# Kernel tuning notes

Hardware: AMD Instinct MI355X
Metric: run time of the kernel (lower is better)

## Reference

```python
import jax, jax.numpy as jnp
import numpy as np

B, T, U, D = 2, 512, 48, 512
H, K = 1024, 128  # hidden_channels, num_classes; fc1 in = 2*D = 1024


def setup_inputs() -> dict:
    key = jax.random.key(0)
    ks = jax.random.split(key, 9)
    s = 0.02
    return {
        "img_feature": jax.random.normal(ks[0], (B, T, D), jnp.float32),
        "label_feature": jax.random.normal(ks[1], (B, U, D), jnp.float32),
        "masks": jnp.ones((B, 1, T), jnp.float32),
        "W1": jax.random.normal(ks[2], (H, 2 * D), jnp.float32) * s,
        "b1": jnp.zeros((H,), jnp.float32),
        "W2": jax.random.normal(ks[3], (K, H), jnp.float32) * s,
        "b2": jnp.zeros((K,), jnp.float32),
        "conv_w": jax.random.normal(ks[4], (K, D), jnp.float32) * s,
        "conv_b": jnp.zeros((K,), jnp.float32),
    }


def reference(img_feature, label_feature, masks, W1, b1, W2, b2, conv_w, conv_b):
    # pointwise Conv1d over img features: (B,T,D) -> (B,K,T), masked
    img_seg_score = (jnp.einsum('btd,kd->bkt', img_feature, conv_w)
                     + conv_b[None, :, None]) * masks
    # fc1(cat(label, img)) == label @ Wl^T + img @ Wi^T + b1 (broadcast add),
    # avoiding the O(B*U*T*2D) repeat+cat intermediate.
    d = label_feature.shape[-1]
    Wl, Wi = W1[:, :d], W1[:, d:]
    lab = jnp.einsum('bud,hd->buh', label_feature, Wl)  # (B,U,H)
    img = jnp.einsum('btd,hd->bth', img_feature, Wi)    # (B,T,H)
    h = jnp.tanh(lab[:, :, None, :] + img[:, None, :, :] + b1)  # (B,U,T,H)
    joint = jnp.einsum('buth,kh->butk', h, W2) + b2
    joint_score = jax.nn.log_softmax(joint, axis=-1)
    return (img_seg_score, joint_score)
```

## Files before the change

kernel.cpp:

```cpp
#include <hip/hip_runtime.h>
#include <math.h>

#define BB 2
#define TT 512
#define UU 48
#define DD 512
#define HH 1024
#define KK 128

typedef _Float16 f16x8 __attribute__((ext_vector_type(8)));
typedef __fp16 fp16x2_t __attribute__((ext_vector_type(2)));
typedef float floatx4 __attribute__((ext_vector_type(4)));

__device__ __forceinline__ f16x8 tanh8z(f16x8 z) {
    f16x8 o;
#pragma unroll
    for (int i = 0; i < 8; i += 2) {
        float e0 = __builtin_amdgcn_exp2f((float)z[i]);
        float e1 = __builtin_amdgcn_exp2f((float)z[i + 1]);
        float r0 = __builtin_amdgcn_rcpf(e0 + 1.0f);
        float r1 = __builtin_amdgcn_rcpf(e1 + 1.0f);
        fp16x2_t p = __builtin_amdgcn_cvt_pkrtz(fmaf(-2.0f, r0, 1.0f),
                                                fmaf(-2.0f, r1, 1.0f));
        o[i] = (_Float16)p[0];
        o[i + 1] = (_Float16)p[1];
    }
    return o;
}

__global__ __launch_bounds__(256) void mid_kernel5(
    const float* __restrict__ img, const float* __restrict__ labf,
    const float* __restrict__ W1, const float* __restrict__ W2,
    const float* __restrict__ conv_w,
    const float* __restrict__ b1, const float* __restrict__ conv_b,
    const float* __restrict__ masks,
    _Float16* __restrict__ imgHf, _Float16* __restrict__ labHf,
    _Float16* __restrict__ W2s, float* __restrict__ seg_out) {
    int bid = blockIdx.x, tid = threadIdx.x;
    if (bid >= 624) {
        int base = (bid - 624) * 256 + tid;
#pragma unroll
        for (int i = 0; i < 32; ++i) {
            int o = base + i * 4096;
            int hg = o >> 10, kk2 = (o >> 3) & 127, hl = o & 7;
            W2s[o] = (_Float16)W2[(size_t)kk2 * HH + hg * 8 + hl];
        }
        return;
    }
    __shared__ __align__(16) _Float16 a_s[32][72];
    __shared__ __align__(16) _Float16 w_s[4096];
    const float* Arow;
    const float* Wbase;
    int r0, n0b, wstride, region;
    if (bid < 512) {
        region = 0; Arow = img; Wbase = W1 + 512; wstride = 2 * DD;
        int xcd = bid & 7, j = bid >> 3;
        r0 = (j & 31) * 32; n0b = (xcd * 2 + (j >> 5)) * 64;
    } else if (bid < 560) {
        region = 1; Arow = labf; Wbase = W1; wstride = 2 * DD;
        int i = bid - 512; r0 = (i % 3) * 32; n0b = (i / 3) * 64;
    } else {
        region = 2; Arow = img; Wbase = conv_w; wstride = DD;
        int i = bid - 560; r0 = (i >> 1) * 32; n0b = (i & 1) * 64;
    }
    int lane = tid & 63, wv = tid >> 6;
    int m0 = (wv & 1) * 16, n0w = (wv >> 1) * 32;
    int q = lane >> 4, r = lane & 15;
    int arow = tid >> 3, acol = (tid & 7) * 8;
    int wn = tid >> 2, wk0 = (tid & 3) * 16;
    const float* aptr = &Arow[(size_t)(r0 + arow) * DD + acol];
    const float* wptr = &Wbase[(size_t)(n0b + wn) * wstride + wk0];
    floatx4 acc[2] = {};
    float4 pa0, pa1, pw[4];
    pa0 = *(const float4*)aptr;
    pa1 = *(const float4*)(aptr + 4);
#pragma unroll
    for (int i2 = 0; i2 < 4; ++i2) pw[i2] = *(const float4*)(wptr + i2 * 4);
    for (int c = 0; c < 8; ++c) {
        f16x8 av;
        av[0] = (_Float16)pa0.x; av[1] = (_Float16)pa0.y;
        av[2] = (_Float16)pa0.z; av[3] = (_Float16)pa0.w;
        av[4] = (_Float16)pa1.x; av[5] = (_Float16)pa1.y;
        av[6] = (_Float16)pa1.z; av[7] = (_Float16)pa1.w;
        *(f16x8*)&a_s[arow][acol] = av;
        f16x8 w0, w1;
        w0[0] = (_Float16)pw[0].x; w0[1] = (_Float16)pw[0].y;
        w0[2] = (_Float16)pw[0].z; w0[3] = (_Float16)pw[0].w;
        w0[4] = (_Float16)pw[1].x; w0[5] = (_Float16)pw[1].y;
        w0[6] = (_Float16)pw[1].z; w0[7] = (_Float16)pw[1].w;
        w1[0] = (_Float16)pw[2].x; w1[1] = (_Float16)pw[2].y;
        w1[2] = (_Float16)pw[2].z; w1[3] = (_Float16)pw[2].w;
        w1[4] = (_Float16)pw[3].x; w1[5] = (_Float16)pw[3].y;
        w1[6] = (_Float16)pw[3].z; w1[7] = (_Float16)pw[3].w;
        int kg = wk0 >> 3;
        *(f16x8*)&w_s[((kg + 0) * 64 + wn) * 8] = w0;
        *(f16x8*)&w_s[((kg + 1) * 64 + wn) * 8] = w1;
        __syncthreads();
        if (c < 7) {
            int cb = (c + 1) * 64;
            pa0 = *(const float4*)(aptr + cb);
            pa1 = *(const float4*)(aptr + cb + 4);
#pragma unroll
            for (int i2 = 0; i2 < 4; ++i2)
                pw[i2] = *(const float4*)(wptr + cb + i2 * 4);
        }
#pragma unroll
        for (int kt = 0; kt < 2; ++kt) {
            f16x8 af = *(const f16x8*)&a_s[m0 + r][kt * 32 + q * 8];
#pragma unroll
            for (int nt = 0; nt < 2; ++nt) {
                f16x8 bf = *(const f16x8*)
                    &w_s[((kt * 4 + q) * 64 + n0w + nt * 16 + r) * 8];
                acc[nt] = __builtin_amdgcn_mfma_f32_16x16x32_f16(
                    af, bf, acc[nt], 0, 0, 0);
            }
        }
        __syncthreads();
    }
    const float SC = 2.8853900817779268f;
    if (region == 0) {
#pragma unroll
        for (int nt = 0; nt < 2; ++nt) {
            int n = n0b + n0w + nt * 16 + r;
#pragma unroll
            for (int rr = 0; rr < 4; ++rr)
                imgHf[(size_t)(r0 + m0 + 4 * q + rr) * HH + n] =
                    (_Float16)(acc[nt][rr] * SC);
        }
    } else if (region == 1) {
#pragma unroll
        for (int nt = 0; nt < 2; ++nt) {
            int n = n0b + n0w + nt * 16 + r;
            float bv = b1[n];
#pragma unroll
            for (int rr = 0; rr < 4; ++rr)
                labHf[(size_t)(r0 + m0 + 4 * q + rr) * HH + n] =
                    (_Float16)((acc[nt][rr] + bv) * SC);
        }
    } else {
#pragma unroll
        for (int nt = 0; nt < 2; ++nt) {
            int k = n0b + n0w + nt * 16 + r;
            float bv = conv_b[k];
#pragma unroll
            for (int rr = 0; rr < 4; ++rr) {
                int row = r0 + m0 + 4 * q + rr;
                int b = row >> 9, t = row & 511;
                seg_out[((size_t)b * KK + k) * TT + t] =
                    (acc[nt][rr] + bv) * masks[row];
            }
        }
    }
}

__global__ __launch_bounds__(128) void joint_kernel17(
    const _Float16* __restrict__ imgHf,
    const _Float16* __restrict__ labHf,
    const _Float16* __restrict__ W2s,
    const float* __restrict__ b2,
    float* __restrict__ out) {
    __shared__ __align__(16) _Float16 a_s[64][72];
    __shared__ __align__(16) _Float16 w_s[8192];
    __shared__ __align__(16) _Float16 l_s[64];
    int tid = threadIdx.x, bid = blockIdx.x;
    int lane = tid & 63, wm = tid >> 6;
    int ql = lane >> 4, r = lane & 15;
    int g0 = bid * 64;
    int bu = g0 >> 9;
    int tbase = ((bu >= UU) ? TT : 0) + (g0 & 511);
    int arow = tid >> 1, acol = (tid & 1) * 32;
    const _Float16* ap = imgHf + (size_t)(tbase + arow) * HH + acol;
    const _Float16* wq = W2s + (size_t)tid * 8;
    const _Float16* lp = labHf + (size_t)bu * HH;
    int m0 = wm * 32;
    floatx4 acc0[8] = {}, acc1[8] = {};
    f16x8 pa[4], pw[8], plab;
#pragma unroll
    for (int j = 0; j < 4; ++j) pa[j] = *(const f16x8*)(ap + j * 8);
#pragma unroll
    for (int j = 0; j < 8; ++j) pw[j] = *(const f16x8*)(wq + j * 1024);
    if (tid < 8) plab = *(const f16x8*)(lp + tid * 8);
#pragma unroll 1
    for (int c = 0; c < 16; ++c) {
#pragma unroll
        for (int j = 0; j < 4; ++j) *(f16x8*)&a_s[arow][acol + j * 8] = pa[j];
#pragma unroll
        for (int j = 0; j < 8; ++j) *(f16x8*)&w_s[tid * 8 + j * 1024] = pw[j];
        if (tid < 8) *(f16x8*)&l_s[tid * 8] = plab;
        __syncthreads();
        if (c < 15) {
            int cb = (c + 1) * 64;
#pragma unroll
            for (int j = 0; j < 4; ++j)
                pa[j] = *(const f16x8*)(ap + cb + j * 8);
            const _Float16* wc = wq + (size_t)(c + 1) * 8192;
#pragma unroll
            for (int j = 0; j < 8; ++j) pw[j] = *(const f16x8*)(wc + j * 1024);
            if (tid < 8) plab = *(const f16x8*)(lp + cb + tid * 8);
        }
#pragma unroll
        for (int kt = 0; kt < 2; ++kt) {
            f16x8 lf = *(const f16x8*)&l_s[kt * 32 + ql * 8];
            f16x8 af0 = *(const f16x8*)&a_s[m0 + r][kt * 32 + ql * 8];
            f16x8 af1 = *(const f16x8*)&a_s[m0 + 16 + r][kt * 32 + ql * 8];
            f16x8 a0 = tanh8z(af0 + lf);
            f16x8 a1 = tanh8z(af1 + lf);
#pragma unroll
            for (int nt = 0; nt < 8; ++nt) {
                f16x8 bf = *(const f16x8*)
                    &w_s[((kt * 4 + ql) * 128 + nt * 16 + r) * 8];
                acc0[nt] = __builtin_amdgcn_mfma_f32_16x16x32_f16(
                    a0, bf, acc0[nt], 0, 0, 0);
                acc1[nt] = __builtin_amdgcn_mfma_f32_16x16x32_f16(
                    a1, bf, acc1[nt], 0, 0, 0);
            }
        }
        __syncthreads();
    }
    float b2v[8];
#pragma unroll
    for (int nt = 0; nt < 8; ++nt) b2v[nt] = b2[nt * 16 + r];
#pragma unroll
    for (int mt = 0; mt < 2; ++mt) {
#pragma unroll
        for (int rr = 0; rr < 4; ++rr) {
            float v[8];
            float mx = -INFINITY;
#pragma unroll
            for (int nt = 0; nt < 8; ++nt) {
                v[nt] = (mt ? acc1[nt][rr] : acc0[nt][rr]) + b2v[nt];
                mx = fmaxf(mx, v[nt]);
            }
            mx = fmaxf(mx, __shfl_xor(mx, 1, 16));
            mx = fmaxf(mx, __shfl_xor(mx, 2, 16));
            mx = fmaxf(mx, __shfl_xor(mx, 4, 16));
            mx = fmaxf(mx, __shfl_xor(mx, 8, 16));
            float s = 0.f;
#pragma unroll
            for (int nt = 0; nt < 8; ++nt) s += __expf(v[nt] - mx);
            s += __shfl_xor(s, 1, 16);
            s += __shfl_xor(s, 2, 16);
            s += __shfl_xor(s, 4, 16);
            s += __shfl_xor(s, 8, 16);
            float lse = mx + __logf(s);
            float* orow =
                out + (size_t)(g0 + m0 + mt * 16 + 4 * ql + rr) * KK;
#pragma unroll
            for (int nt = 0; nt < 8; ++nt)
                orow[nt * 16 + r] = v[nt] - lse;
        }
    }
}

extern "C" void kernel_launch(void* const* d_in, const int* in_sizes, int n_in,
                              void* d_out, int out_size, void* d_ws, size_t ws_size,
                              hipStream_t stream) {
    const float* img    = (const float*)d_in[0];
    const float* labf   = (const float*)d_in[1];
    const float* masks  = (const float*)d_in[2];
    const float* W1     = (const float*)d_in[3];
    const float* b1     = (const float*)d_in[4];
    const float* W2     = (const float*)d_in[5];
    const float* b2     = (const float*)d_in[6];
    const float* conv_w = (const float*)d_in[7];
    const float* conv_b = (const float*)d_in[8];
    float* out = (float*)d_out;

    _Float16* base  = (_Float16*)d_ws;
    _Float16* imgHf = base;
    _Float16* labHf = imgHf + 1024 * 1024;
    _Float16* W2s   = labHf + 96 * 1024;

    mid_kernel5<<<640, 256, 0, stream>>>(img, labf, W1, W2, conv_w,
                                         b1, conv_b, masks,
                                         imgHf, labHf, W2s, out);
    joint_kernel17<<<768, 128, 0, stream>>>(imgHf, labHf, W2s, b2,
                                            out + (size_t)BB * KK * TT);
}
```

Baseline: 124.9 us.

## Split H reduction across wave pairs in joint kernel with LDS reduction

Doubles the joint kernel block to 256 threads. Each pair of waves splits the hidden dimension in half, with each half processing 512 H columns over 8 iterations instead of 16. Partial accumulators are then exchanged through shared memory and summed, and each wave finishes the log-softmax for 16 of its 32 rows. The aim is more waves per tile to hide latency and shorten the serial K-loop, at the cost of double-size shared buffers, an extra LDS reduction and lower per-block occupancy.

```diff
diff --git a/kernel.cpp b/kernel.cpp
--- a/kernel.cpp
+++ b/kernel.cpp
@@ -153,62 +153,81 @@
     }
 }
 
-__global__ __launch_bounds__(128) void joint_kernel17(
+__global__ __launch_bounds__(256) void joint_kernel19(
     const _Float16* __restrict__ imgHf,
     const _Float16* __restrict__ labHf,
     const _Float16* __restrict__ W2s,
     const float* __restrict__ b2,
     float* __restrict__ out) {
-    __shared__ __align__(16) _Float16 a_s[64][72];
-    __shared__ __align__(16) _Float16 w_s[8192];
-    __shared__ __align__(16) _Float16 l_s[64];
+    __shared__ __align__(16) _Float16 a_s[2][64][72];
+    __shared__ __align__(16) _Float16 w_s[2][8192];
+    __shared__ __align__(16) _Float16 l_s[2][64];
     int tid = threadIdx.x, bid = blockIdx.x;
-    int lane = tid & 63, wm = tid >> 6;
+    int lane = tid & 63, wv = tid >> 6;
+    int rg = wv >> 1, hh = wv & 1;
     int ql = lane >> 4, r = lane & 15;
     int g0 = bid * 64;
     int bu = g0 >> 9;
     int tbase = ((bu >= UU) ? TT : 0) + (g0 & 511);
-    int arow = tid >> 1, acol = (tid & 1) * 32;
-    const _Float16* ap = imgHf + (size_t)(tbase + arow) * HH + acol;
-    const _Float16* wq = W2s + (size_t)tid * 8;
+    int arow = tid >> 2, acol = (tid & 3) * 16;
+    const _Float16* ap0 = imgHf + (size_t)(tbase + arow) * HH + acol;
+    const _Float16* ap1 = ap0 + 512;
     const _Float16* lp = labHf + (size_t)bu * HH;
-    int m0 = wm * 32;
+    int m0r = rg * 32;
     floatx4 acc0[8] = {}, acc1[8] = {};
-    f16x8 pa[4], pw[8], plab;
-#pragma unroll
-    for (int j = 0; j < 4; ++j) pa[j] = *(const f16x8*)(ap + j * 8);
-#pragma unroll
-    for (int j = 0; j < 8; ++j) pw[j] = *(const f16x8*)(wq + j * 1024);
-    if (tid < 8) plab = *(const f16x8*)(lp + tid * 8);
+    f16x8 pa00, pa01, pa10, pa11;
+    f16x8 pw0[4], pw1[4], plab;
+    pa00 = *(const f16x8*)ap0;  pa01 = *(const f16x8*)(ap0 + 8);
+    pa10 = *(const f16x8*)ap1;  pa11 = *(const f16x8*)(ap1 + 8);
+#pragma unroll
+    for (int j = 0; j < 4; ++j) {
+        pw0[j] = *(const f16x8*)(W2s + (size_t)0 * 8192 + tid * 8 + j * 2048);
+        pw1[j] = *(const f16x8*)(W2s + (size_t)8 * 8192 + tid * 8 + j * 2048);
+    }
+    if (tid < 16)
+        plab = *(const f16x8*)(lp + (tid >> 3) * 512 + (tid & 7) * 8);
 #pragma unroll 1
-    for (int c = 0; c < 16; ++c) {
-#pragma unroll
-        for (int j = 0; j < 4; ++j) *(f16x8*)&a_s[arow][acol + j * 8] = pa[j];
-#pragma unroll
-        for (int j = 0; j < 8; ++j) *(f16x8*)&w_s[tid * 8 + j * 1024] = pw[j];
-        if (tid < 8) *(f16x8*)&l_s[tid * 8] = plab;
-        __syncthreads();
-        if (c < 15) {
-            int cb = (c + 1) * 64;
-#pragma unroll
-            for (int j = 0; j < 4; ++j)
-                pa[j] = *(const f16x8*)(ap + cb + j * 8);
-            const _Float16* wc = wq + (size_t)(c + 1) * 8192;
-#pragma unroll
-            for (int j = 0; j < 8; ++j) pw[j] = *(const f16x8*)(wc + j * 1024);
-            if (tid < 8) plab = *(const f16x8*)(lp + cb + tid * 8);
+    for (int t = 0; t < 8; ++t) {
+        *(f16x8*)&a_s[0][arow][acol] = pa00;
+        *(f16x8*)&a_s[0][arow][acol + 8] = pa01;
+        *(f16x8*)&a_s[1][arow][acol] = pa10;
+        *(f16x8*)&a_s[1][arow][acol + 8] = pa11;
+#pragma unroll
+        for (int j = 0; j < 4; ++j) {
+            *(f16x8*)&w_s[0][tid * 8 + j * 2048] = pw0[j];
+            *(f16x8*)&w_s[1][tid * 8 + j * 2048] = pw1[j];
+        }
+        if (tid < 16) *(f16x8*)&l_s[tid >> 3][(tid & 7) * 8] = plab;
+        __syncthreads();
+        if (t < 7) {
+            int cb = (t + 1) * 64;
+            pa00 = *(const f16x8*)(ap0 + cb);
+            pa01 = *(const f16x8*)(ap0 + cb + 8);
+            pa10 = *(const f16x8*)(ap1 + cb);
+            pa11 = *(const f16x8*)(ap1 + cb + 8);
+#pragma unroll
+            for (int j = 0; j < 4; ++j) {
+                pw0[j] = *(const f16x8*)(W2s + (size_t)(t + 1) * 8192 +
+                                         tid * 8 + j * 2048);
+                pw1[j] = *(const f16x8*)(W2s + (size_t)(t + 9) * 8192 +
+                                         tid * 8 + j * 2048);
+            }
+            if (tid < 16)
+                plab = *(const f16x8*)(lp + (tid >> 3) * 512 + cb +
+                                       (tid & 7) * 8);
         }
 #pragma unroll
         for (int kt = 0; kt < 2; ++kt) {
-            f16x8 lf = *(const f16x8*)&l_s[kt * 32 + ql * 8];
-            f16x8 af0 = *(const f16x8*)&a_s[m0 + r][kt * 32 + ql * 8];
-            f16x8 af1 = *(const f16x8*)&a_s[m0 + 16 + r][kt * 32 + ql * 8];
+            f16x8 lf = *(const f16x8*)&l_s[hh][kt * 32 + ql * 8];
+            f16x8 af0 = *(const f16x8*)&a_s[hh][m0r + r][kt * 32 + ql * 8];
+            f16x8 af1 =
+                *(const f16x8*)&a_s[hh][m0r + 16 + r][kt * 32 + ql * 8];
             f16x8 a0 = tanh8z(af0 + lf);
             f16x8 a1 = tanh8z(af1 + lf);
 #pragma unroll
             for (int nt = 0; nt < 8; ++nt) {
                 f16x8 bf = *(const f16x8*)
-                    &w_s[((kt * 4 + ql) * 128 + nt * 16 + r) * 8];
+                    &w_s[hh][((kt * 4 + ql) * 128 + nt * 16 + r) * 8];
                 acc0[nt] = __builtin_amdgcn_mfma_f32_16x16x32_f16(
                     a0, bf, acc0[nt], 0, 0, 0);
                 acc1[nt] = __builtin_amdgcn_mfma_f32_16x16x32_f16(
@@ -217,38 +236,49 @@
         }
         __syncthreads();
     }
+    {
+        float* red = (float*)w_s;
+        float* myout = red + (size_t)wv * 2048;
+#pragma unroll
+        for (int nt = 0; nt < 8; ++nt)
+            *(floatx4*)&myout[nt * 256 + lane * 4] = hh ? acc0[nt] : acc1[nt];
+        __syncthreads();
+        float* other = red + (size_t)(wv ^ 1) * 2048;
+#pragma unroll
+        for (int nt = 0; nt < 8; ++nt) {
+            floatx4 v = *(const floatx4*)&other[nt * 256 + lane * 4];
+            if (hh) acc1[nt] += v; else acc0[nt] += v;
+        }
+    }
     float b2v[8];
 #pragma unroll
     for (int nt = 0; nt < 8; ++nt) b2v[nt] = b2[nt * 16 + r];
 #pragma unroll
-    for (int mt = 0; mt < 2; ++mt) {
-#pragma unroll
-        for (int rr = 0; rr < 4; ++rr) {
-            float v[8];
-            float mx = -INFINITY;
-#pragma unroll
-            for (int nt = 0; nt < 8; ++nt) {
-                v[nt] = (mt ? acc1[nt][rr] : acc0[nt][rr]) + b2v[nt];
-                mx = fmaxf(mx, v[nt]);
-            }
-            mx = fmaxf(mx, __shfl_xor(mx, 1, 16));
-            mx = fmaxf(mx, __shfl_xor(mx, 2, 16));
-            mx = fmaxf(mx, __shfl_xor(mx, 4, 16));
-            mx = fmaxf(mx, __shfl_xor(mx, 8, 16));
-            float s = 0.f;
-#pragma unroll
-            for (int nt = 0; nt < 8; ++nt) s += __expf(v[nt] - mx);
-            s += __shfl_xor(s, 1, 16);
-            s += __shfl_xor(s, 2, 16);
-            s += __shfl_xor(s, 4, 16);
-            s += __shfl_xor(s, 8, 16);
-            float lse = mx + __logf(s);
-            float* orow =
-                out + (size_t)(g0 + m0 + mt * 16 + 4 * ql + rr) * KK;
-#pragma unroll
-            for (int nt = 0; nt < 8; ++nt)
-                orow[nt * 16 + r] = v[nt] - lse;
-        }
+    for (int rr = 0; rr < 4; ++rr) {
+        float v[8];
+        float mx = -INFINITY;
+#pragma unroll
+        for (int nt = 0; nt < 8; ++nt) {
+            v[nt] = (hh ? acc1[nt][rr] : acc0[nt][rr]) + b2v[nt];
+            mx = fmaxf(mx, v[nt]);
+        }
+        mx = fmaxf(mx, __shfl_xor(mx, 1, 16));
+        mx = fmaxf(mx, __shfl_xor(mx, 2, 16));
+        mx = fmaxf(mx, __shfl_xor(mx, 4, 16));
+        mx = fmaxf(mx, __shfl_xor(mx, 8, 16));
+        float s = 0.f;
+#pragma unroll
+        for (int nt = 0; nt < 8; ++nt) s += __expf(v[nt] - mx);
+        s += __shfl_xor(s, 1, 16);
+        s += __shfl_xor(s, 2, 16);
+        s += __shfl_xor(s, 4, 16);
+        s += __shfl_xor(s, 8, 16);
+        float lse = mx + __logf(s);
+        float* orow =
+            out + (size_t)(g0 + m0r + hh * 16 + 4 * ql + rr) * KK;
+#pragma unroll
+        for (int nt = 0; nt < 8; ++nt)
+            orow[nt * 16 + r] = v[nt] - lse;
     }
 }
 
@@ -274,6 +304,6 @@
     mid_kernel5<<<640, 256, 0, stream>>>(img, labf, W1, W2, conv_w,
                                          b1, conv_b, masks,
                                          imgHf, labHf, W2s, out);
-    joint_kernel17<<<768, 128, 0, stream>>>(imgHf, labHf, W2s, b2,
+    joint_kernel19<<<768, 256, 0, stream>>>(imgHf, labHf, W2s, b2,
                                             out + (size_t)BB * KK * TT);
 }
```

Result: faster. 118.8 us (-4.9%).
